# Kernel optimization log

Hardware: AMD Instinct MI355X
Metric: run time of the kernel (lower is better)

The kernel has to match this reference:

```python
import jax, jax.numpy as jnp
import numpy as np

DIM = 64  # matches init kwarg `dim`; temperature = sqrt(DIM)


def setup_inputs() -> dict:
    key = jax.random.key(0)
    kq, kk, kv = jax.random.split(key, 3)
    B, Lq, Lk, d = 16, 4096, 4096, DIM
    q = jax.random.normal(kq, (B, Lq, d), dtype=jnp.float32)
    k = jax.random.normal(kk, (B, Lk, d), dtype=jnp.float32)
    v = jax.random.normal(kv, (B, Lk, d), dtype=jnp.float32)
    return {"q": q, "k": k, "v": v}


def reference(q, k, v):
    # attn = softmax(q @ k^T / sqrt(dim)); dropout is identity in eval mode.
    temperature = jnp.asarray(np.sqrt(DIM), dtype=q.dtype)
    scores = jnp.einsum('bqd,bkd->bqk', q, k) / temperature  # [B, Lq, Lk]
    attn = jax.nn.softmax(scores, axis=-1)
    out = jnp.einsum('bqk,bkd->bqd', attn, v)  # [B, Lq, d]
    return out
```

## Files before the change

kernel.cpp:

```cpp
#include <hip/hip_runtime.h>
#include <stdint.h>
#include <math.h>

typedef __attribute__((ext_vector_type(2)))  float f2;
typedef __attribute__((ext_vector_type(4)))  float f4;
typedef __attribute__((ext_vector_type(16))) float f32x16;
typedef __attribute__((ext_vector_type(8)))  short bf16x8;

#define NB   16
#define LSEQ 4096
#define DH   64
#define QB   256
#define KVB  64
#define NT   (LSEQ / KVB)
#define NR   (NT / 2)
#define TSZ  (KVB * DH)

__device__ __forceinline__ short f2bf(float f) {
    union { float f; uint32_t u; } v; v.f = f;
    return (short)((v.u + 0x7FFFu + ((v.u >> 16) & 1u)) >> 16);
}

__device__ __forceinline__ uint32_t cvtpk(float lo, float hi) {
    uint32_t r;
    asm("v_cvt_pk_bf16_f32 %0, %1, %2" : "=v"(r) : "v"(lo), "v"(hi));
    return r;
}

__global__ __launch_bounds__(512, 2) void fa_fwd(
    const float* __restrict__ Q, const float* __restrict__ K,
    const float* __restrict__ V, float* __restrict__ O)
{
    __shared__ __align__(16) short smem[16 * TSZ];
    __shared__ float lscr[4][64];
    short* const k_base = smem;
    short* const v_base = smem + 8 * TSZ;

    const int tid  = threadIdx.x;
    const int lane = tid & 63;
    const int wv   = tid >> 6;
    const int qsub = wv & 3;
    const int par  = wv >> 2;
    const int l31  = lane & 31;
    const int H    = lane >> 5;

    const int bid  = blockIdx.x;
    const int xcd  = bid & 7;
    const int slot = bid >> 3;
    const int b    = xcd * 2 + (slot >> 4);
    const int qt   = slot & 15;
    const int q0   = qt * QB + qsub * 64;

    const float* Qb = Q + (size_t)b * LSEQ * DH;
    const float* Kb = K + (size_t)b * LSEQ * DH;
    const float* Vb = V + (size_t)b * LSEQ * DH;
    float*       Ob = O + (size_t)b * LSEQ * DH;

    const float QS = 0.125f * 1.44269504088896340736f;

    bf16x8 qfA[4], qfB[4];
#pragma unroll
    for (int kb = 0; kb < 4; ++kb) {
#pragma unroll
        for (int g = 0; g < 2; ++g) {
            const float* src = Qb + (size_t)(q0 + 32 * g + l31) * DH + 16 * kb + 8 * H;
            f4 a = *(const f4*)src;
            f4 c = *(const f4*)(src + 4);
            bf16x8 f;
            f[0] = f2bf(a[0] * QS); f[1] = f2bf(a[1] * QS);
            f[2] = f2bf(a[2] * QS); f[3] = f2bf(a[3] * QS);
            f[4] = f2bf(c[0] * QS); f[5] = f2bf(c[1] * QS);
            f[6] = f2bf(c[2] * QS); f[7] = f2bf(c[3] * QS);
            if (g == 0) qfA[kb] = f; else qfB[kb] = f;
        }
    }

    const int sid  = tid & 255;
    const int ssel = tid >> 8;
    f4 kreg[4];
    f2 vreg[8];
    const int k_kv0 = sid >> 3;
    const int k_d0  = (sid & 7) * 8;
    const int v_d0  = (sid & 31) * 2;
    const int v_g   = sid >> 5;

#define LOADK(T0)                                                               \
    {                                                                           \
        const int kv0 = ((T0) + ssel) * KVB;                                    \
        _Pragma("unroll")                                                       \
        for (int p = 0; p < 2; ++p) {                                           \
            const float* src = Kb + (size_t)(kv0 + k_kv0 + 32 * p) * DH + k_d0; \
            kreg[2 * p]     = *(const f4*)src;                                  \
            kreg[2 * p + 1] = *(const f4*)(src + 4);                            \
        }                                                                       \
        _Pragma("unroll")                                                       \
        for (int j = 0; j < 8; ++j)                                             \
            vreg[j] = *(const f2*)&Vb[(size_t)(kv0 + 8 * v_g + j) * DH + v_d0]; \
    }

#define WRITEK(T0)                                                              \
    {                                                                           \
        const int bw = ((T0) + ssel) & 7;                                       \
        _Pragma("unroll")                                                       \
        for (int p = 0; p < 2; ++p) {                                           \
            const int kv = k_kv0 + 32 * p;                                      \
            union { bf16x8 v; uint32_t u[4]; } t;                               \
            t.u[0] = cvtpk(kreg[2 * p][0], kreg[2 * p][1]);                     \
            t.u[1] = cvtpk(kreg[2 * p][2], kreg[2 * p][3]);                     \
            t.u[2] = cvtpk(kreg[2 * p + 1][0], kreg[2 * p + 1][1]);             \
            t.u[3] = cvtpk(kreg[2 * p + 1][2], kreg[2 * p + 1][3]);             \
            *(bf16x8*)&k_base[bw * TSZ + kv * DH + (k_d0 ^ ((kv & 7) << 3))] = t.v; \
        }                                                                       \
        _Pragma("unroll")                                                       \
        for (int c = 0; c < 2; ++c) {                                           \
            const int d = v_d0 + c;                                             \
            union { bf16x8 v; uint32_t u[4]; } t;                               \
            t.u[0] = cvtpk(vreg[0][c], vreg[1][c]);                             \
            t.u[1] = cvtpk(vreg[2][c], vreg[3][c]);                             \
            t.u[2] = cvtpk(vreg[4][c], vreg[5][c]);                             \
            t.u[3] = cvtpk(vreg[6][c], vreg[7][c]);                             \
            *(bf16x8*)&v_base[bw * TSZ + d * KVB + 8 * (v_g ^ (d & 7))] = t.v;  \
        }                                                                       \
    }

#define QK2(BUF)                                                                \
    {                                                                           \
        _Pragma("unroll")                                                       \
        for (int i = 0; i < 16; ++i) { sA0[i] = 0.f; sA1[i] = 0.f; sB0[i] = 0.f; sB1[i] = 0.f; } \
        _Pragma("unroll")                                                       \
        for (int kb = 0; kb < 4; ++kb) {                                        \
            const int d0 = 16 * kb + 8 * H;                                     \
            bf16x8 kf0 = *(const bf16x8*)&k_base[(BUF) * TSZ + (l31)      * DH + (d0 ^ ((l31 & 7) << 3))]; \
            bf16x8 kf1 = *(const bf16x8*)&k_base[(BUF) * TSZ + (32 + l31) * DH + (d0 ^ ((l31 & 7) << 3))]; \
            sA0 = __builtin_amdgcn_mfma_f32_32x32x16_bf16(kf0, qfA[kb], sA0, 0, 0, 0); \
            sB0 = __builtin_amdgcn_mfma_f32_32x32x16_bf16(kf0, qfB[kb], sB0, 0, 0, 0); \
            sA1 = __builtin_amdgcn_mfma_f32_32x32x16_bf16(kf1, qfA[kb], sA1, 0, 0, 0); \
            sB1 = __builtin_amdgcn_mfma_f32_32x32x16_bf16(kf1, qfB[kb], sB1, 0, 0, 0); \
        }                                                                       \
    }

#define EXPSUM(S, L)                                                            \
    {                                                                           \
        float r0 = 0.f, r1 = 0.f, r2 = 0.f, r3 = 0.f;                           \
        _Pragma("unroll")                                                       \
        for (int i = 0; i < 4; ++i) {                                           \
            S[i]      = __builtin_amdgcn_exp2f(S[i]);      r0 += S[i];          \
            S[i + 4]  = __builtin_amdgcn_exp2f(S[i + 4]);  r1 += S[i + 4];      \
            S[i + 8]  = __builtin_amdgcn_exp2f(S[i + 8]);  r2 += S[i + 8];      \
            S[i + 12] = __builtin_amdgcn_exp2f(S[i + 12]); r3 += S[i + 12];     \
        }                                                                       \
        L += (r0 + r1) + (r2 + r3);                                             \
    }

#define MAKE_PA(P, ks2, dst)                                                    \
    {                                                                           \
        uint32_t a1 = cvtpk(P[8*(ks2)+0], P[8*(ks2)+1]);                        \
        uint32_t b1 = cvtpk(P[8*(ks2)+4], P[8*(ks2)+5]);                        \
        uint32_t a2 = cvtpk(P[8*(ks2)+2], P[8*(ks2)+3]);                        \
        uint32_t b2 = cvtpk(P[8*(ks2)+6], P[8*(ks2)+7]);                        \
        asm volatile("v_permlane32_swap_b32 %0, %1" : "+v"(a1), "+v"(b1));      \
        asm volatile("v_permlane32_swap_b32 %0, %1" : "+v"(a2), "+v"(b2));      \
        union { bf16x8 v; uint32_t u[4]; } t;                                   \
        t.u[0] = a1; t.u[1] = a2; t.u[2] = b1; t.u[3] = b2;                     \
        dst = t.v;                                                              \
    }

#define PVKS2(BUF, ks, pA, pB)                                                  \
    {                                                                           \
        const int d0g = 2 * (ks) + H;                                           \
        bf16x8 vf0 = *(const bf16x8*)&v_base[(BUF) * TSZ + (l31)      * KVB + 8 * (d0g ^ (l31 & 7))]; \
        bf16x8 vf1 = *(const bf16x8*)&v_base[(BUF) * TSZ + (32 + l31) * KVB + 8 * (d0g ^ (l31 & 7))]; \
        oA0 = __builtin_amdgcn_mfma_f32_32x32x16_bf16(vf0, pA, oA0, 0, 0, 0);   \
        oB0 = __builtin_amdgcn_mfma_f32_32x32x16_bf16(vf0, pB, oB0, 0, 0, 0);   \
        oA1 = __builtin_amdgcn_mfma_f32_32x32x16_bf16(vf1, pA, oA1, 0, 0, 0);   \
        oB1 = __builtin_amdgcn_mfma_f32_32x32x16_bf16(vf1, pB, oB1, 0, 0, 0);   \
    }

#define BODY(R, DO_LOAD, DO_STAGE)                                              \
    {                                                                           \
        const int cb = (2 * (R) + par) & 7;                                     \
        bf16x8 pa0, pa1, pb0, pb1, pa2, pa3, pb2, pb3;                          \
        EXPSUM(sA0, lA); MAKE_PA(sA0, 0, pa0); MAKE_PA(sA0, 1, pa1);            \
        EXPSUM(sB0, lB); MAKE_PA(sB0, 0, pb0); MAKE_PA(sB0, 1, pb1);            \
        EXPSUM(sA1, lA); MAKE_PA(sA1, 0, pa2); MAKE_PA(sA1, 1, pa3);            \
        EXPSUM(sB1, lB); MAKE_PA(sB1, 0, pb2); MAKE_PA(sB1, 1, pb3);            \
        if (DO_STAGE) {                                                         \
            WRITEK(2 * (R) + 2);                                                \
            __syncthreads();                                                    \
            if (DO_LOAD) LOADK(2 * (R) + 4);                                    \
            const int nb = (2 * (R) + 2 + par) & 7;                             \
            __builtin_amdgcn_s_setprio(1);                                      \
            QK2(nb);                                                            \
            __builtin_amdgcn_s_setprio(0);                                      \
        }                                                                       \
        __builtin_amdgcn_s_setprio(1);                                          \
        PVKS2(cb, 0, pa0, pb0); PVKS2(cb, 1, pa1, pb1);                         \
        PVKS2(cb, 2, pa2, pb2); PVKS2(cb, 3, pa3, pb3);                         \
        __builtin_amdgcn_s_setprio(0);                                          \
    }

    f32x16 oA0, oA1, oB0, oB1;
#pragma unroll
    for (int i = 0; i < 16; ++i) { oA0[i] = 0.f; oA1[i] = 0.f; oB0[i] = 0.f; oB1[i] = 0.f; }
    float lA = 0.f, lB = 0.f;

    LOADK(0);
    WRITEK(0);
    __syncthreads();
    LOADK(2);

    f32x16 sA0, sA1, sB0, sB1;
    QK2(par);

    for (int r = 0; r < NR - 2; ++r) BODY(r, 1, 1);
    BODY(NR - 2, 0, 1);
    BODY(NR - 1, 0, 0);

    lA += __shfl_xor(lA, 32);
    lB += __shfl_xor(lB, 32);
    __syncthreads();
    float* const oscr = (float*)smem;
    if (par == 1) {
        const int rowA = qsub * 64 + l31;
        const int rowB = qsub * 64 + 32 + l31;
#pragma unroll
        for (int i = 0; i < 16; ++i) {
            const int d = (i & 3) + 8 * (i >> 2) + 4 * H;
            oscr[rowA * 64 + ((d      + rowA) & 63)] = oA0[i];
            oscr[rowA * 64 + ((d + 32 + rowA) & 63)] = oA1[i];
            oscr[rowB * 64 + ((d      + rowB) & 63)] = oB0[i];
            oscr[rowB * 64 + ((d + 32 + rowB) & 63)] = oB1[i];
        }
        if (H == 0) { lscr[qsub][l31] = lA; lscr[qsub][32 + l31] = lB; }
    }
    __syncthreads();
    if (par == 0) {
        const int rowA = qsub * 64 + l31;
        const int rowB = qsub * 64 + 32 + l31;
        const float invA = 1.0f / (lA + lscr[qsub][l31]);
        const float invB = 1.0f / (lB + lscr[qsub][32 + l31]);
        const int qA = q0 + l31;
        const int qB = q0 + 32 + l31;
#pragma unroll
        for (int k = 0; k < 4; ++k) {
            f4 a0, a1, b0, b1;
#pragma unroll
            for (int m = 0; m < 4; ++m) {
                const int d = m + 8 * k + 4 * H;
                a0[m] = (oA0[4*k+m] + oscr[rowA * 64 + ((d      + rowA) & 63)]) * invA;
                a1[m] = (oA1[4*k+m] + oscr[rowA * 64 + ((d + 32 + rowA) & 63)]) * invA;
                b0[m] = (oB0[4*k+m] + oscr[rowB * 64 + ((d      + rowB) & 63)]) * invB;
                b1[m] = (oB1[4*k+m] + oscr[rowB * 64 + ((d + 32 + rowB) & 63)]) * invB;
            }
            *(f4*)&Ob[(size_t)qA * DH +      8 * k + 4 * H] = a0;
            *(f4*)&Ob[(size_t)qA * DH + 32 + 8 * k + 4 * H] = a1;
            *(f4*)&Ob[(size_t)qB * DH +      8 * k + 4 * H] = b0;
            *(f4*)&Ob[(size_t)qB * DH + 32 + 8 * k + 4 * H] = b1;
        }
    }
#undef LOADK
#undef WRITEK
#undef QK2
#undef EXPSUM
#undef MAKE_PA
#undef PVKS2
#undef BODY
}

extern "C" void kernel_launch(void* const* d_in, const int* in_sizes, int n_in,
                              void* d_out, int out_size, void* d_ws, size_t ws_size,
                              hipStream_t stream) {
    (void)in_sizes; (void)n_in; (void)d_ws; (void)ws_size; (void)out_size;
    const float* q = (const float*)d_in[0];
    const float* k = (const float*)d_in[1];
    const float* v = (const float*)d_in[2];
    float* o = (float*)d_out;
    hipLaunchKernelGGL(fa_fwd, dim3(NB * (LSEQ / QB)), dim3(512), 0, stream, q, k, v, o);
}
```

Measured before the change: 90.78 us.

## Restructure per-warp-parity schedule: split softmax/PV for even, defer PV for odd warps

Replaces the uniform loop body with a per-parity schedule. Even warps compute QK on the current tile, then interleave exp/pack with PV in two halves. Odd warps run the PV of the previous tile (kept in registers) before the softmax of the current one. The intent is to desynchronise MFMA and exp/VALU phases between warp groups so they overlap on the SIMD. In exchange, odd warps keep extra bf16 P registers across iterations, which raises register pressure, and the code adds divergent branches and a tail PV step.

```diff
diff --git a/kernel.cpp b/kernel.cpp
--- a/kernel.cpp
+++ b/kernel.cpp
@@ -176,33 +176,49 @@
         oB1 = __builtin_amdgcn_mfma_f32_32x32x16_bf16(vf1, pB, oB1, 0, 0, 0);   \
     }
 
-#define BODY(R, DO_LOAD, DO_STAGE)                                              \
-    {                                                                           \
-        const int cb = (2 * (R) + par) & 7;                                     \
-        bf16x8 pa0, pa1, pb0, pb1, pa2, pa3, pb2, pb3;                          \
-        EXPSUM(sA0, lA); MAKE_PA(sA0, 0, pa0); MAKE_PA(sA0, 1, pa1);            \
-        EXPSUM(sB0, lB); MAKE_PA(sB0, 0, pb0); MAKE_PA(sB0, 1, pb1);            \
-        EXPSUM(sA1, lA); MAKE_PA(sA1, 0, pa2); MAKE_PA(sA1, 1, pa3);            \
-        EXPSUM(sB1, lB); MAKE_PA(sB1, 0, pb2); MAKE_PA(sB1, 1, pb3);            \
+#define SEG(R, DO_LOAD, DO_STAGE)                                               \
+    {                                                                           \
+        const int tslot = (2 * (R) + par) & 7;                                  \
+        __builtin_amdgcn_s_setprio(1);                                          \
+        QK2(tslot);                                                             \
+        __builtin_amdgcn_s_setprio(0);                                          \
+        if (par == 0) {                                                         \
+            bf16x8 pa0, pa1, pb0, pb1;                                          \
+            EXPSUM(sA0, lA); MAKE_PA(sA0, 0, pa0); MAKE_PA(sA0, 1, pa1);        \
+            EXPSUM(sB0, lB); MAKE_PA(sB0, 0, pb0); MAKE_PA(sB0, 1, pb1);        \
+            __builtin_amdgcn_s_setprio(1);                                      \
+            PVKS2(tslot, 0, pa0, pb0); PVKS2(tslot, 1, pa1, pb1);               \
+            __builtin_amdgcn_s_setprio(0);                                      \
+            EXPSUM(sA1, lA); MAKE_PA(sA1, 0, pa0); MAKE_PA(sA1, 1, pa1);        \
+            EXPSUM(sB1, lB); MAKE_PA(sB1, 0, pb0); MAKE_PA(sB1, 1, pb1);        \
+            __builtin_amdgcn_s_setprio(1);                                      \
+            PVKS2(tslot, 2, pa0, pb0); PVKS2(tslot, 3, pa1, pb1);               \
+            __builtin_amdgcn_s_setprio(0);                                      \
+        } else {                                                                \
+            if ((R) > 0) {                                                      \
+                const int pslot = (2 * (R) - 1) & 7;                            \
+                __builtin_amdgcn_s_setprio(1);                                  \
+                PVKS2(pslot, 0, ppA00, ppB00); PVKS2(pslot, 1, ppA01, ppB01);   \
+                PVKS2(pslot, 2, ppA10, ppB10); PVKS2(pslot, 3, ppA11, ppB11);   \
+                __builtin_amdgcn_s_setprio(0);                                  \
+            }                                                                   \
+            EXPSUM(sA0, lA); MAKE_PA(sA0, 0, ppA00); MAKE_PA(sA0, 1, ppA01);    \
+            EXPSUM(sB0, lB); MAKE_PA(sB0, 0, ppB00); MAKE_PA(sB0, 1, ppB01);    \
+            EXPSUM(sA1, lA); MAKE_PA(sA1, 0, ppA10); MAKE_PA(sA1, 1, ppA11);    \
+            EXPSUM(sB1, lB); MAKE_PA(sB1, 0, ppB10); MAKE_PA(sB1, 1, ppB11);    \
+        }                                                                       \
         if (DO_STAGE) {                                                         \
             WRITEK(2 * (R) + 2);                                                \
             __syncthreads();                                                    \
             if (DO_LOAD) LOADK(2 * (R) + 4);                                    \
-            const int nb = (2 * (R) + 2 + par) & 7;                             \
-            __builtin_amdgcn_s_setprio(1);                                      \
-            QK2(nb);                                                            \
-            __builtin_amdgcn_s_setprio(0);                                      \
-        }                                                                       \
-        __builtin_amdgcn_s_setprio(1);                                          \
-        PVKS2(cb, 0, pa0, pb0); PVKS2(cb, 1, pa1, pb1);                         \
-        PVKS2(cb, 2, pa2, pb2); PVKS2(cb, 3, pa3, pb3);                         \
-        __builtin_amdgcn_s_setprio(0);                                          \
+        }                                                                       \
     }
 
     f32x16 oA0, oA1, oB0, oB1;
 #pragma unroll
     for (int i = 0; i < 16; ++i) { oA0[i] = 0.f; oA1[i] = 0.f; oB0[i] = 0.f; oB1[i] = 0.f; }
     float lA = 0.f, lB = 0.f;
+    bf16x8 ppA00, ppA01, ppA10, ppA11, ppB00, ppB01, ppB10, ppB11;
 
     LOADK(0);
     WRITEK(0);
@@ -210,11 +226,17 @@
     LOADK(2);
 
     f32x16 sA0, sA1, sB0, sB1;
-    QK2(par);
-
-    for (int r = 0; r < NR - 2; ++r) BODY(r, 1, 1);
-    BODY(NR - 2, 0, 1);
-    BODY(NR - 1, 0, 0);
+
+    for (int r = 0; r < NR - 2; ++r) SEG(r, 1, 1);
+    SEG(NR - 2, 0, 1);
+    SEG(NR - 1, 0, 0);
+
+    if (par == 1) {
+        __builtin_amdgcn_s_setprio(1);
+        PVKS2((NT - 1) & 7, 0, ppA00, ppB00); PVKS2((NT - 1) & 7, 1, ppA01, ppB01);
+        PVKS2((NT - 1) & 7, 2, ppA10, ppB10); PVKS2((NT - 1) & 7, 3, ppA11, ppB11);
+        __builtin_amdgcn_s_setprio(0);
+    }
 
     lA += __shfl_xor(lA, 32);
     lB += __shfl_xor(lB, 32);
@@ -264,7 +286,7 @@
 #undef EXPSUM
 #undef MAKE_PA
 #undef PVKS2
-#undef BODY
+#undef SEG
 }
 
 extern "C" void kernel_launch(void* const* d_in, const int* in_sizes, int n_in,
```

Result: slower. 157.4 us (+73.4%).
